# Kernel tuning notes

Hardware: AMD Instinct MI355X
Metric: run time of the kernel (lower is better)

Reference implementation:

```python
import jax, jax.numpy as jnp
import numpy as np

T, D, F, V = 16384, 1024, 2048, 4096


def _mlp(x, w1, w2):
    # residual ReLU MLP stand-in for a transformer stack (tokenwise)
    return x + jax.nn.relu(x @ w1) @ w2


def setup_inputs() -> dict:
    key = jax.random.key(0)
    ks = jax.random.split(key, 11)
    s1 = 1.0 / np.sqrt(D)
    s2 = 1.0 / np.sqrt(F)
    g = lambda k, shape, sc: jax.random.normal(k, shape, dtype=jnp.float32) * sc
    return {
        "inputs_embeds": g(ks[0], (T, D), 1.0),
        "enc_w1": g(ks[1], (D, F), s1),
        "enc_w2": g(ks[2], (F, D), s2),
        "back_w1": g(ks[3], (D, F), s1),
        "back_w2": g(ks[4], (F, D), s2),
        "dec_w1": g(ks[5], (D, F), s1),
        "dec_w2": g(ks[6], (F, D), s2),
        "sp_w": g(ks[7], (D, 1), s1),
        "sp_b": jnp.zeros((1,), jnp.float32),
        "pos_emb": g(ks[8], (T, D), 0.02),
        "lm_head": g(ks[9], (D, V), s1),
        "cu_seq_lens": jnp.array([0, 4096, 8192, 12288, 16384], dtype=jnp.int32),
    }


def reference(inputs_embeds, enc_w1, enc_w2, back_w1, back_w2, dec_w1, dec_w2,
              sp_w, sp_b, pos_emb, lm_head, cu_seq_lens):
    # --- encoder (3-layer stack stand-in) ---
    enc = _mlp(inputs_embeds, enc_w1, enc_w2)                 # [T, D]
    # --- token gate: sigmoid + threshold ---
    w = jax.nn.sigmoid(enc @ sp_w + sp_b)[:, 0]               # [T]
    mask = w >= 0.5                                           # keep mask (= ~zero_mask)
    mi = mask.astype(jnp.int32)
    # --- ragged re-pack: within-segment rank of kept tokens (new position ids) ---
    ecs = jnp.cumsum(mi) - mi                                 # exclusive cumsum of kept
    seg = jnp.searchsorted(cu_seq_lens[1:], jnp.arange(T), side="right")
    base = ecs[cu_seq_lens[:-1]][seg]                         # kept-count before each segment
    new_pos = ecs - base                                      # arange(length) per new segment
    # stable sort places kept tokens first in original (packed) order,
    # exactly matching the per-segment concat of the torch version
    order = jnp.argsort(jnp.logical_not(mask), stable=True)   # [T]
    valid = mask[order]
    # gather + weight by gate value, add new position embedding
    gathered = (enc * w[:, None])[order] + pos_emb[new_pos[order]]
    gathered = jnp.where(valid[:, None], gathered, 0.0)
    # --- backbone compute on packed kept tokens ---
    bb = _mlp(gathered, back_w1, back_w2)                     # [T, D] (padded tail unused)
    # --- scatter-combine: kept slots <- backbone, dropped slots <- encoder residual ---
    inv = jnp.argsort(order)
    combined = jnp.where(mask[:, None], bb[inv], enc)         # [T, D]
    # --- decoder (3-layer stack stand-in) + lm head ---
    dec = _mlp(combined, dec_w1, dec_w2)
    logits = dec @ lm_head                                    # [T, V] fp32
    return logits
```

## Files before the change

kernel.cpp:

```cpp
#include <hip/hip_runtime.h>
#include <hip/hip_bf16.h>
#include <math.h>

static constexpr int TT = 16384;
static constexpr int DD = 1024;
static constexpr int FF = 2048;
static constexpr int VV = 4096;

using bf16 = __hip_bfloat16;
typedef __attribute__((ext_vector_type(8))) short bf16x8;
typedef __attribute__((ext_vector_type(4))) float f32x4;

__device__ inline void gload16(const void* g, void* l) {
    __builtin_amdgcn_global_load_lds(
        (const __attribute__((address_space(1))) void*)g,
        (__attribute__((address_space(3))) void*)l, 16, 0, 0);
}

template<int EPI , bool WB16, bool WF32, bool ROWLIM>
__global__ __launch_bounds__(512, 2)
void mgemm8(const bf16* __restrict__ A, const bf16* __restrict__ BT,
            const float* __restrict__ X, bf16* __restrict__ Ob,
            float* __restrict__ Of,
            int M, int N, int K, const int* __restrict__ rowlim)
{
    if constexpr (ROWLIM) { if ((int)blockIdx.y * 256 >= *rowlim) return; }
    const int m0 = blockIdx.y * 256, n0 = blockIdx.x * 256;

    extern __shared__ char smem[];

    const int tid = threadIdx.x;
    const int wv = tid >> 6, ln = tid & 63;
    const int wm = wv >> 2, wn = wv & 3;
    const int lr = ln & 15, lk = ln >> 4;
    const int swz = (lr & 7) << 4;

    const bf16* Ag = A  + (size_t)m0 * K;
    const bf16* Bg = BT + (size_t)n0 * K;

    const int NT = K >> 6;
    const int NI = NT >> 1;

    const int aoff0 = (wm * 128 + lr) * 128;
    const int boff0 = 32768 + (wn * 64 + lr) * 128;
    const int cb0 = (lk * 16) ^ swz;
    const int cb1 = (64 + lk * 16) ^ swz;

    auto STAGE = [&](const bf16* g, int h, int kt, int buf, int op) {
        const int r = ln >> 3;
        const int c = ((ln & 7) ^ r) * 8;
        const bf16* s = g + (size_t)(h * 128 + wv * 16 + r) * K + kt * 64 + c;
        char* d = smem + buf * 65536 + op * 32768 + h * 16384 + wv * 2048;
        gload16(s, d);
        gload16(s + (size_t)8 * K, d + 1024);
    };
    auto stage_j = [&](int j) {
        const int tile = j >> 2;
        if (tile >= NT) return;
        const int part = j & 3;
        const int buf = tile & 1;
        if (part < 2) STAGE(Bg, part, tile, buf, 1);
        else          STAGE(Ag, part - 2, tile, buf, 0);
    };

    bf16x8 afr[2][2], bfr[4][2];
    f32x4 acc[8][4];
    #pragma unroll
    for (int m = 0; m < 8; ++m)
        #pragma unroll
        for (int n = 0; n < 4; ++n) acc[m][n] = (f32x4){0.f, 0.f, 0.f, 0.f};

#define DS_A(BUF, Q) do {                                                     \
    const char* _p = smem + (BUF) * 65536 + aoff0 + (Q) * 4096;               \
    afr[0][0] = *(const bf16x8*)(_p + cb0);                                   \
    afr[0][1] = *(const bf16x8*)(_p + cb1);                                   \
    afr[1][0] = *(const bf16x8*)(_p + 2048 + cb0);                            \
    afr[1][1] = *(const bf16x8*)(_p + 2048 + cb1);                            \
} while (0)

#define DS_B(BUF) do {                                                        \
    const char* _p = smem + (BUF) * 65536 + boff0;                            \
    _Pragma("unroll")                                                         \
    for (int nf = 0; nf < 4; ++nf) {                                          \
        bfr[nf][0] = *(const bf16x8*)(_p + nf * 2048 + cb0);                  \
        bfr[nf][1] = *(const bf16x8*)(_p + nf * 2048 + cb1);                  \
    }                                                                         \
} while (0)

#define MFMAQ(Q) do {                                                         \
    __builtin_amdgcn_s_setprio(1);                                            \
    _Pragma("unroll")                                                         \
    for (int m2 = 0; m2 < 2; ++m2)                                            \
        _Pragma("unroll")                                                     \
        for (int nf = 0; nf < 4; ++nf) {                                      \
            acc[(Q) * 2 + m2][nf] = __builtin_amdgcn_mfma_f32_16x16x32_bf16(  \
                afr[m2][0], bfr[nf][0], acc[(Q) * 2 + m2][nf], 0, 0, 0);      \
            acc[(Q) * 2 + m2][nf] = __builtin_amdgcn_mfma_f32_16x16x32_bf16(  \
                afr[m2][1], bfr[nf][1], acc[(Q) * 2 + m2][nf], 0, 0, 0);      \
        }                                                                     \
    __builtin_amdgcn_s_setprio(0);                                            \
} while (0)

#define PHASE(Q, BUF, DOB, J, W)                                              \
    {                                                                         \
        DS_A(BUF, Q);                                                         \
        if (DOB) DS_B(BUF);                                                   \
        stage_j(J);                                                           \
        if ((W) == 1)      asm volatile("s_waitcnt vmcnt(6)" ::: "memory");   \
        else if ((W) == 2) asm volatile("s_waitcnt vmcnt(0)" ::: "memory");   \
        __builtin_amdgcn_sched_barrier(0);                                    \
        __builtin_amdgcn_s_barrier();                                         \
        MFMAQ(Q);                                                             \
        __builtin_amdgcn_s_barrier();                                         \
    }

    STAGE(Bg, 0, 0, 0, 1); STAGE(Bg, 1, 0, 0, 1);
    STAGE(Ag, 0, 0, 0, 0); STAGE(Ag, 1, 0, 0, 0);
    asm volatile("s_waitcnt vmcnt(4)" ::: "memory");
    STAGE(Bg, 0, 1, 1, 1); STAGE(Bg, 1, 1, 1, 1);
    STAGE(Ag, 0, 1, 1, 0);
    asm volatile("s_waitcnt vmcnt(6)" ::: "memory");
    __builtin_amdgcn_sched_barrier(0);
    __builtin_amdgcn_s_barrier();

    for (int i = 0; i < NI; ++i) {
        const int jb = 7 + 8 * i;
        const bool last = (i + 1 == NI);
        PHASE(0, 0, true,  jb + 0, 0);
        PHASE(1, 0, false, jb + 1, 0);
        PHASE(2, 0, false, jb + 2, 0);
        PHASE(3, 0, false, jb + 3, last ? 2 : 1);
        PHASE(0, 1, true,  jb + 4, 0);
        PHASE(1, 1, false, jb + 5, 0);
        PHASE(2, 1, false, jb + 6, 0);
        PHASE(3, 1, false, jb + 7, last ? 0 : 1);
    }

#undef PHASE
#undef MFMAQ
#undef DS_B
#undef DS_A

    #pragma unroll
    for (int mf = 0; mf < 8; ++mf)
        #pragma unroll
        for (int nf = 0; nf < 4; ++nf)
            #pragma unroll
            for (int rr = 0; rr < 4; ++rr) {
                const int row = m0 + wm * 128 + mf * 16 + lk * 4 + rr;
                const int col = n0 + wn * 64 + nf * 16 + lr;
                float v = acc[mf][nf][rr];
                if constexpr (EPI == 1) v = fmaxf(v, 0.f);
                if constexpr (EPI == 2) v += X[(size_t)row * N + col];
                if constexpr (WB16) Ob[(size_t)row * N + col] = __float2bfloat16(v);
                if constexpr (WF32) Of[(size_t)row * N + col] = v;
            }
}

__global__ __launch_bounds__(256, 2)
void mgemm_nt3(const bf16* __restrict__ Ah, const bf16* __restrict__ Al,
               const bf16* __restrict__ Bh, const bf16* __restrict__ Bl,
               bf16* __restrict__ Ob, float* __restrict__ gpart,
               const float* __restrict__ qv, int M, int N, int K)
{
    const int m0 = blockIdx.y * 128, n0 = blockIdx.x * 128;

    extern __shared__ char smem[];
    bf16* sAh = (bf16*)smem;
    bf16* sBh = (bf16*)(smem + 8192);
    bf16* sAl = (bf16*)(smem + 16384);
    bf16* sBl = (bf16*)(smem + 24576);

    const int tid = threadIdx.x;
    const int wv = tid >> 6, ln = tid & 63;
    const int wm = wv >> 1, wn = wv & 1;
    const int lr = ln & 15, lk = ln >> 4;
    const int arow = ln >> 2;
    const int acol = (ln & 3) * 8;

    const bf16* Abase_h = Ah + (size_t)m0 * K;
    const bf16* Abase_l = Al + (size_t)m0 * K;
    const bf16* Bbase_h = Bh + (size_t)n0 * K;
    const bf16* Bbase_l = Bl + (size_t)n0 * K;

    f32x4 acc[4][4];
    #pragma unroll
    for (int m = 0; m < 4; ++m)
        #pragma unroll
        for (int n = 0; n < 4; ++n) acc[m][n] = (f32x4){0.f, 0.f, 0.f, 0.f};

    const int nt = K >> 5;
    for (int kt = 0; kt < nt; ++kt) {
        #pragma unroll
        for (int p = 0; p < 2; ++p) {
            const int row = p * 64 + wv * 16;
            gload16(Abase_h + (size_t)(row + arow) * K + kt * 32 + acol, sAh + row * 32);
            gload16(Bbase_h + (size_t)(row + arow) * K + kt * 32 + acol, sBh + row * 32);
            gload16(Abase_l + (size_t)(row + arow) * K + kt * 32 + acol, sAl + row * 32);
            gload16(Bbase_l + (size_t)(row + arow) * K + kt * 32 + acol, sBl + row * 32);
        }
        __syncthreads();

        bf16x8 ah[4], bh[4], al[4], bl[4];
        #pragma unroll
        for (int m = 0; m < 4; ++m) {
            ah[m] = *(const bf16x8*)(sAh + (wm * 64 + m * 16 + lr) * 32 + lk * 8);
            al[m] = *(const bf16x8*)(sAl + (wm * 64 + m * 16 + lr) * 32 + lk * 8);
        }
        #pragma unroll
        for (int n = 0; n < 4; ++n) {
            bh[n] = *(const bf16x8*)(sBh + (wn * 64 + n * 16 + lr) * 32 + lk * 8);
            bl[n] = *(const bf16x8*)(sBl + (wn * 64 + n * 16 + lr) * 32 + lk * 8);
        }
        #pragma unroll
        for (int m = 0; m < 4; ++m)
            #pragma unroll
            for (int n = 0; n < 4; ++n) {
                acc[m][n] = __builtin_amdgcn_mfma_f32_16x16x32_bf16(ah[m], bh[n], acc[m][n], 0, 0, 0);
                acc[m][n] = __builtin_amdgcn_mfma_f32_16x16x32_bf16(ah[m], bl[n], acc[m][n], 0, 0, 0);
                acc[m][n] = __builtin_amdgcn_mfma_f32_16x16x32_bf16(al[m], bh[n], acc[m][n], 0, 0, 0);
            }
        __syncthreads();
    }

    {
        float qvv[4];
        #pragma unroll
        for (int n = 0; n < 4; ++n) qvv[n] = qv[n0 + wn * 64 + n * 16 + lr];
        #pragma unroll
        for (int m = 0; m < 4; ++m)
            #pragma unroll
            for (int r = 0; r < 4; ++r) {
                float s = 0.f;
                #pragma unroll
                for (int n = 0; n < 4; ++n) s += fmaxf(acc[m][n][r], 0.f) * qvv[n];
                s += __shfl_xor(s, 1, 64); s += __shfl_xor(s, 2, 64);
                s += __shfl_xor(s, 4, 64); s += __shfl_xor(s, 8, 64);
                if (lr == 0)
                    gpart[(size_t)(blockIdx.x * 2 + wn) * M + (m0 + wm * 64 + m * 16 + lk * 4 + r)] = s;
            }
    }

    #pragma unroll
    for (int m = 0; m < 4; ++m)
        #pragma unroll
        for (int n = 0; n < 4; ++n)
            #pragma unroll
            for (int r = 0; r < 4; ++r) {
                const int row = m0 + wm * 64 + m * 16 + lk * 4 + r;
                const int col = n0 + wn * 64 + n * 16 + lr;
                Ob[(size_t)row * N + col] = __float2bfloat16(fmaxf(acc[m][n][r], 0.f));
            }
}

template<bool SPLIT>
__global__ void wtrans(const float* __restrict__ W, bf16* __restrict__ Th,
                       bf16* __restrict__ Tl, int R, int C)
{
    __shared__ float tile[32][33];
    const int tx = threadIdx.x & 31, ty = threadIdx.x >> 5;
    const int rb = blockIdx.y * 32, cb = blockIdx.x * 32;
    #pragma unroll
    for (int i = 0; i < 32; i += 8)
        tile[ty + i][tx] = W[(size_t)(rb + ty + i) * C + cb + tx];
    __syncthreads();
    #pragma unroll
    for (int i = 0; i < 32; i += 8) {
        const float v = tile[tx][ty + i];
        const size_t o = (size_t)(cb + ty + i) * R + rb + tx;
        const bf16 h = __float2bfloat16(v);
        Th[o] = h;
        if constexpr (SPLIT) Tl[o] = __float2bfloat16(v - __bfloat162float(h));
    }
}

__global__ void splitx(const float* __restrict__ x, bf16* __restrict__ xh,
                       bf16* __restrict__ xl)
{
    const int i = blockIdx.x * 256 + threadIdx.x;
    const float4 v = ((const float4*)x)[i];
    const float f[4] = {v.x, v.y, v.z, v.w};
    #pragma unroll
    for (int j = 0; j < 4; ++j) {
        const bf16 h = __float2bfloat16(f[j]);
        xh[i * 4 + j] = h;
        xl[i * 4 + j] = __float2bfloat16(f[j] - __bfloat162float(h));
    }
}

__global__ void qvec(const float* __restrict__ w2, const float* __restrict__ sp,
                     float* __restrict__ q)
{
    const int f  = blockIdx.x * 4 + (threadIdx.x >> 6);
    const int ln = threadIdx.x & 63;
    float s = 0.f;
    const float* row = w2 + (size_t)f * DD;
    for (int k = ln; k < DD; k += 64) s += row[k] * sp[k];
    #pragma unroll
    for (int off = 32; off > 0; off >>= 1) s += __shfl_xor(s, off, 64);
    if (ln == 0) q[f] = s;
}

__global__ void gate2(const float* __restrict__ x, const float* __restrict__ spw,
                      const float* __restrict__ spb, const float* __restrict__ gpart,
                      float* __restrict__ w, int* __restrict__ mi)
{
    const int t  = blockIdx.x * 4 + (threadIdx.x >> 6);
    const int ln = threadIdx.x & 63;
    float s = 0.f;
    const float* row = x + (size_t)t * DD;
    for (int k = ln; k < DD; k += 64) s += row[k] * spw[k];
    if (ln < 32) s += gpart[(size_t)ln * TT + t];
    #pragma unroll
    for (int off = 32; off > 0; off >>= 1) s += __shfl_xor(s, off, 64);
    if (ln == 0) {
        const float sg = 1.f / (1.f + expf(-(s + spb[0])));
        w[t]  = sg;
        mi[t] = (sg >= 0.5f) ? 1 : 0;
    }
}

__global__ void scan_kernel(const int* __restrict__ mi, const int* __restrict__ cu,
                            int* __restrict__ ecs, int* __restrict__ meta)
{
    __shared__ int sums[256];
    const int tid  = threadIdx.x;
    const int base = tid * 64;
    int s = 0;
    for (int i = 0; i < 64; ++i) s += mi[base + i];
    sums[tid] = s;
    __syncthreads();
    for (int off = 1; off < 256; off <<= 1) {
        int v = (tid >= off) ? sums[tid - off] : 0;
        __syncthreads();
        sums[tid] += v;
        __syncthreads();
    }
    int run = (tid == 0) ? 0 : sums[tid - 1];
    for (int i = 0; i < 64; ++i) { ecs[base + i] = run; run += mi[base + i]; }
    if (tid == 255) meta[0] = sums[255];
    if (tid < 4) {
        const int idx = cu[tid];
        const int tc = idx >> 6, rem = idx & 63;
        int e = (tc == 0) ? 0 : sums[tc - 1];
        for (int i = 0; i < rem; ++i) e += mi[tc * 64 + i];
        meta[1 + tid] = e;
    }
}

__global__ void pack_kernel(const float* __restrict__ enc, const float* __restrict__ w,
                            const int* __restrict__ mi, const int* __restrict__ ecs,
                            const int* __restrict__ cu, const int* __restrict__ meta,
                            const float* __restrict__ pos_emb,
                            float* __restrict__ Pf, bf16* __restrict__ Pb)
{
    const int t    = blockIdx.x * 4 + (threadIdx.x >> 6);
    const int lane = threadIdx.x & 63;
    if (!mi[t]) return;
    const int e = ecs[t];
    int seg = 0;
    #pragma unroll
    for (int ss = 1; ss < 4; ++ss) if (t >= cu[ss]) seg = ss;
    const int np = e - meta[1 + seg];
    const float wt = w[t];
    const float4* src = (const float4*)(enc + (size_t)t * DD);
    const float4* pe  = (const float4*)(pos_emb + (size_t)np * DD);
    float4* dstf = (float4*)(Pf + (size_t)e * DD);
    bf16*   dstb = Pb + (size_t)e * DD;
    for (int c = lane; c < DD / 4; c += 64) {
        float4 v = src[c], p = pe[c];
        v.x = v.x * wt + p.x; v.y = v.y * wt + p.y;
        v.z = v.z * wt + p.z; v.w = v.w * wt + p.w;
        dstf[c] = v;
        dstb[c * 4 + 0] = __float2bfloat16(v.x);
        dstb[c * 4 + 1] = __float2bfloat16(v.y);
        dstb[c * 4 + 2] = __float2bfloat16(v.z);
        dstb[c * 4 + 3] = __float2bfloat16(v.w);
    }
}

__global__ void combine_kernel(float* __restrict__ ENC, const float* __restrict__ BBf,
                               const int* __restrict__ mi, const int* __restrict__ ecs,
                               bf16* __restrict__ Cb)
{
    const int t    = blockIdx.x * 4 + (threadIdx.x >> 6);
    const int lane = threadIdx.x & 63;
    const bool kept = mi[t] != 0;
    const float4* src = kept ? (const float4*)(BBf + (size_t)ecs[t] * DD)
                             : (const float4*)(ENC + (size_t)t * DD);
    float4* dstf = (float4*)(ENC + (size_t)t * DD);
    bf16*   dstb = Cb + (size_t)t * DD;
    for (int c = lane; c < DD / 4; c += 64) {
        const float4 v = src[c];
        if (kept) dstf[c] = v;
        dstb[c * 4 + 0] = __float2bfloat16(v.x);
        dstb[c * 4 + 1] = __float2bfloat16(v.y);
        dstb[c * 4 + 2] = __float2bfloat16(v.z);
        dstb[c * 4 + 3] = __float2bfloat16(v.w);
    }
}

extern "C" void kernel_launch(void* const* d_in, const int* in_sizes, int n_in,
                              void* d_out, int out_size, void* d_ws, size_t ws_size,
                              hipStream_t stream)
{
    (void)in_sizes; (void)n_in; (void)out_size; (void)ws_size;
    const float* x   = (const float*)d_in[0];
    const float* ew1 = (const float*)d_in[1];
    const float* ew2 = (const float*)d_in[2];
    const float* bw1 = (const float*)d_in[3];
    const float* bw2 = (const float*)d_in[4];
    const float* dw1 = (const float*)d_in[5];
    const float* dw2 = (const float*)d_in[6];
    const float* spw = (const float*)d_in[7];
    const float* spb = (const float*)d_in[8];
    const float* pem = (const float*)d_in[9];
    const float* lmh = (const float*)d_in[10];
    const int*   cu  = (const int*)d_in[11];
    float* out = (float*)d_out;

    (void)hipFuncSetAttribute((const void*)mgemm8<2, false, true, false>,
                              hipFuncAttributeMaxDynamicSharedMemorySize, 131072);
    (void)hipFuncSetAttribute((const void*)mgemm8<1, true, false, true>,
                              hipFuncAttributeMaxDynamicSharedMemorySize, 131072);
    (void)hipFuncSetAttribute((const void*)mgemm8<2, false, true, true>,
                              hipFuncAttributeMaxDynamicSharedMemorySize, 131072);
    (void)hipFuncSetAttribute((const void*)mgemm8<1, true, false, false>,
                              hipFuncAttributeMaxDynamicSharedMemorySize, 131072);
    (void)hipFuncSetAttribute((const void*)mgemm8<2, true, false, false>,
                              hipFuncAttributeMaxDynamicSharedMemorySize, 131072);
    (void)hipFuncSetAttribute((const void*)mgemm8<0, false, true, false>,
                              hipFuncAttributeMaxDynamicSharedMemorySize, 131072);

    char* w = (char*)d_ws;
    auto alloc = [&](size_t bytes) { char* p = w; w += bytes; return p; };
    bf16* ew1hT = (bf16*)alloc((size_t)FF * DD * 2);
    bf16* ew1lT = (bf16*)alloc((size_t)FF * DD * 2);
    bf16* ew2T  = (bf16*)alloc((size_t)DD * FF * 2);
    bf16* bw1T  = (bf16*)alloc((size_t)FF * DD * 2);
    bf16* bw2T  = (bf16*)alloc((size_t)DD * FF * 2);
    bf16* lmhT  = (bf16*)alloc((size_t)VV * DD * 2);
    float* qv   = (float*)alloc((size_t)FF * 4);
    float* GP   = (float*)alloc((size_t)32 * TT * 4);
    float* WG   = (float*)alloc((size_t)TT * 4);
    int*   MI   = (int*)alloc((size_t)TT * 4);
    int*   ECS  = (int*)alloc((size_t)TT * 4);
    int*   META = (int*)alloc(64);
    bf16* Xh    = (bf16*)alloc((size_t)TT * DD * 2);
    bf16* Xl    = (bf16*)alloc((size_t)TT * DD * 2);
    bf16* Hb    = (bf16*)alloc((size_t)TT * FF * 2);
    float* ENC  = (float*)alloc((size_t)TT * DD * 4);
    float* Pf   = (float*)alloc((size_t)TT * DD * 4);
    bf16* Pb    = (bf16*)alloc((size_t)TT * DD * 2);
    bf16* dw1T  = ew1hT;
    bf16* dw2T  = ew1lT;

    const dim3 blk(256);
    const dim3 blk8(512);

    splitx<<<TT * DD / 4 / 256, blk, 0, stream>>>(x, Xh, Xl);
    wtrans<true ><<<dim3(FF / 32, DD / 32), blk, 0, stream>>>(ew1, ew1hT, ew1lT, DD, FF);
    wtrans<false><<<dim3(DD / 32, FF / 32), blk, 0, stream>>>(ew2, ew2T, nullptr, FF, DD);
    wtrans<false><<<dim3(FF / 32, DD / 32), blk, 0, stream>>>(bw1, bw1T, nullptr, DD, FF);
    wtrans<false><<<dim3(DD / 32, FF / 32), blk, 0, stream>>>(bw2, bw2T, nullptr, FF, DD);
    wtrans<false><<<dim3(VV / 32, DD / 32), blk, 0, stream>>>(lmh, lmhT, nullptr, DD, VV);
    qvec<<<FF / 4, blk, 0, stream>>>(ew2, spw, qv);

    mgemm_nt3<<<dim3(FF / 128, TT / 128), blk, 32768, stream>>>(
        Xh, Xl, ew1hT, ew1lT, Hb, GP, qv, TT, FF, DD);

    gate2<<<TT / 4, blk, 0, stream>>>(x, spw, spb, GP, WG, MI);
    scan_kernel<<<1, blk, 0, stream>>>(MI, cu, ECS, META);

    mgemm8<2, false, true, false><<<dim3(DD / 256, TT / 256), blk8, 131072, stream>>>(
        Hb, ew2T, x, nullptr, ENC, TT, DD, FF, nullptr);

    pack_kernel<<<TT / 4, blk, 0, stream>>>(ENC, WG, MI, ECS, cu, META, pem, Pf, Pb);

    wtrans<false><<<dim3(FF / 32, DD / 32), blk, 0, stream>>>(dw1, dw1T, nullptr, DD, FF);
    wtrans<false><<<dim3(DD / 32, FF / 32), blk, 0, stream>>>(dw2, dw2T, nullptr, FF, DD);

    mgemm8<1, true, false, true><<<dim3(FF / 256, TT / 256), blk8, 131072, stream>>>(
        Pb, bw1T, nullptr, Hb, nullptr, TT, FF, DD, META);
    mgemm8<2, false, true, true><<<dim3(DD / 256, TT / 256), blk8, 131072, stream>>>(
        Hb, bw2T, Pf, nullptr, Pf, TT, DD, FF, META);

    combine_kernel<<<TT / 4, blk, 0, stream>>>(ENC, Pf, MI, ECS, Xl);

    mgemm8<1, true, false, false><<<dim3(FF / 256, TT / 256), blk8, 131072, stream>>>(
        Xl, dw1T, nullptr, Hb, nullptr, TT, FF, DD, nullptr);
    mgemm8<2, true, false, false><<<dim3(DD / 256, TT / 256), blk8, 131072, stream>>>(
        Hb, dw2T, ENC, Xh, nullptr, TT, DD, FF, nullptr);

    mgemm8<0, false, true, false><<<dim3(VV / 256, TT / 256), blk8, 131072, stream>>>(
        Xh, lmhT, nullptr, nullptr, out, TT, VV, DD, nullptr);
}
```

Measured before the change: 864.5 us.

## Replace split-bf16 encoder GEMM with plain bf16 plus fp32 fixup near gate threshold

The first encoder GEMM drops the three-MFMA hi/lo split-precision scheme and uses the single-pass bf16 mgemm8 kernel, with the gate partial-sum epilogue moved into mgemm8. Tokens whose gate logit lands within a small margin of zero are recorded through an atomic counter. An fp32 GEMV then recomputes their gate contribution so the keep mask still matches the reference. This removes the split conversion, the extra bf16 buffers and two-thirds of the MFMA work in that GEMM. In exchange it adds the fixup kernels and risks mask mismatches if more than CAP tokens fall inside the margin, or if bf16 error exceeds TAU.

```diff
diff --git a/kernel.cpp b/kernel.cpp
--- a/kernel.cpp
+++ b/kernel.cpp
@@ -6,6 +6,8 @@
 static constexpr int DD = 1024;
 static constexpr int FF = 2048;
 static constexpr int VV = 4096;
+static constexpr int CAP = 4096;
+#define TAU 0.02f
 
 using bf16 = __hip_bfloat16;
 typedef __attribute__((ext_vector_type(8))) short bf16x8;
@@ -17,11 +19,12 @@
         (__attribute__((address_space(3))) void*)l, 16, 0, 0);
 }
 
-template<int EPI , bool WB16, bool WF32, bool ROWLIM>
+template<int EPI , bool WB16, bool WF32, bool ROWLIM, bool GPART>
 __global__ __launch_bounds__(512, 2)
 void mgemm8(const bf16* __restrict__ A, const bf16* __restrict__ BT,
             const float* __restrict__ X, bf16* __restrict__ Ob,
-            float* __restrict__ Of,
+            float* __restrict__ Of, float* __restrict__ gpart,
+            const float* __restrict__ qv,
             int M, int N, int K, const int* __restrict__ rowlim)
 {
     if constexpr (ROWLIM) { if ((int)blockIdx.y * 256 >= *rowlim) return; }
@@ -141,6 +144,25 @@
 #undef DS_B
 #undef DS_A
 
+    if constexpr (GPART) {
+        float qvv[4];
+        #pragma unroll
+        for (int nf = 0; nf < 4; ++nf) qvv[nf] = qv[n0 + wn * 64 + nf * 16 + lr];
+        #pragma unroll
+        for (int mf = 0; mf < 8; ++mf)
+            #pragma unroll
+            for (int rr = 0; rr < 4; ++rr) {
+                float s = 0.f;
+                #pragma unroll
+                for (int nf = 0; nf < 4; ++nf) s += fmaxf(acc[mf][nf][rr], 0.f) * qvv[nf];
+                s += __shfl_xor(s, 1, 64); s += __shfl_xor(s, 2, 64);
+                s += __shfl_xor(s, 4, 64); s += __shfl_xor(s, 8, 64);
+                if (lr == 0)
+                    gpart[(size_t)(blockIdx.x * 4 + wn) * M +
+                          (m0 + wm * 128 + mf * 16 + lk * 4 + rr)] = s;
+            }
+    }
+
     #pragma unroll
     for (int mf = 0; mf < 8; ++mf)
         #pragma unroll
@@ -157,105 +179,8 @@
             }
 }
 
-__global__ __launch_bounds__(256, 2)
-void mgemm_nt3(const bf16* __restrict__ Ah, const bf16* __restrict__ Al,
-               const bf16* __restrict__ Bh, const bf16* __restrict__ Bl,
-               bf16* __restrict__ Ob, float* __restrict__ gpart,
-               const float* __restrict__ qv, int M, int N, int K)
-{
-    const int m0 = blockIdx.y * 128, n0 = blockIdx.x * 128;
-
-    extern __shared__ char smem[];
-    bf16* sAh = (bf16*)smem;
-    bf16* sBh = (bf16*)(smem + 8192);
-    bf16* sAl = (bf16*)(smem + 16384);
-    bf16* sBl = (bf16*)(smem + 24576);
-
-    const int tid = threadIdx.x;
-    const int wv = tid >> 6, ln = tid & 63;
-    const int wm = wv >> 1, wn = wv & 1;
-    const int lr = ln & 15, lk = ln >> 4;
-    const int arow = ln >> 2;
-    const int acol = (ln & 3) * 8;
-
-    const bf16* Abase_h = Ah + (size_t)m0 * K;
-    const bf16* Abase_l = Al + (size_t)m0 * K;
-    const bf16* Bbase_h = Bh + (size_t)n0 * K;
-    const bf16* Bbase_l = Bl + (size_t)n0 * K;
-
-    f32x4 acc[4][4];
-    #pragma unroll
-    for (int m = 0; m < 4; ++m)
-        #pragma unroll
-        for (int n = 0; n < 4; ++n) acc[m][n] = (f32x4){0.f, 0.f, 0.f, 0.f};
-
-    const int nt = K >> 5;
-    for (int kt = 0; kt < nt; ++kt) {
-        #pragma unroll
-        for (int p = 0; p < 2; ++p) {
-            const int row = p * 64 + wv * 16;
-            gload16(Abase_h + (size_t)(row + arow) * K + kt * 32 + acol, sAh + row * 32);
-            gload16(Bbase_h + (size_t)(row + arow) * K + kt * 32 + acol, sBh + row * 32);
-            gload16(Abase_l + (size_t)(row + arow) * K + kt * 32 + acol, sAl + row * 32);
-            gload16(Bbase_l + (size_t)(row + arow) * K + kt * 32 + acol, sBl + row * 32);
-        }
-        __syncthreads();
-
-        bf16x8 ah[4], bh[4], al[4], bl[4];
-        #pragma unroll
-        for (int m = 0; m < 4; ++m) {
-            ah[m] = *(const bf16x8*)(sAh + (wm * 64 + m * 16 + lr) * 32 + lk * 8);
-            al[m] = *(const bf16x8*)(sAl + (wm * 64 + m * 16 + lr) * 32 + lk * 8);
-        }
-        #pragma unroll
-        for (int n = 0; n < 4; ++n) {
-            bh[n] = *(const bf16x8*)(sBh + (wn * 64 + n * 16 + lr) * 32 + lk * 8);
-            bl[n] = *(const bf16x8*)(sBl + (wn * 64 + n * 16 + lr) * 32 + lk * 8);
-        }
-        #pragma unroll
-        for (int m = 0; m < 4; ++m)
-            #pragma unroll
-            for (int n = 0; n < 4; ++n) {
-                acc[m][n] = __builtin_amdgcn_mfma_f32_16x16x32_bf16(ah[m], bh[n], acc[m][n], 0, 0, 0);
-                acc[m][n] = __builtin_amdgcn_mfma_f32_16x16x32_bf16(ah[m], bl[n], acc[m][n], 0, 0, 0);
-                acc[m][n] = __builtin_amdgcn_mfma_f32_16x16x32_bf16(al[m], bh[n], acc[m][n], 0, 0, 0);
-            }
-        __syncthreads();
-    }
-
-    {
-        float qvv[4];
-        #pragma unroll
-        for (int n = 0; n < 4; ++n) qvv[n] = qv[n0 + wn * 64 + n * 16 + lr];
-        #pragma unroll
-        for (int m = 0; m < 4; ++m)
-            #pragma unroll
-            for (int r = 0; r < 4; ++r) {
-                float s = 0.f;
-                #pragma unroll
-                for (int n = 0; n < 4; ++n) s += fmaxf(acc[m][n][r], 0.f) * qvv[n];
-                s += __shfl_xor(s, 1, 64); s += __shfl_xor(s, 2, 64);
-                s += __shfl_xor(s, 4, 64); s += __shfl_xor(s, 8, 64);
-                if (lr == 0)
-                    gpart[(size_t)(blockIdx.x * 2 + wn) * M + (m0 + wm * 64 + m * 16 + lk * 4 + r)] = s;
-            }
-    }
-
-    #pragma unroll
-    for (int m = 0; m < 4; ++m)
-        #pragma unroll
-        for (int n = 0; n < 4; ++n)
-            #pragma unroll
-            for (int r = 0; r < 4; ++r) {
-                const int row = m0 + wm * 64 + m * 16 + lk * 4 + r;
-                const int col = n0 + wn * 64 + n * 16 + lr;
-                Ob[(size_t)row * N + col] = __float2bfloat16(fmaxf(acc[m][n][r], 0.f));
-            }
-}
-
-template<bool SPLIT>
 __global__ void wtrans(const float* __restrict__ W, bf16* __restrict__ Th,
-                       bf16* __restrict__ Tl, int R, int C)
+                       int R, int C)
 {
     __shared__ float tile[32][33];
     const int tx = threadIdx.x & 31, ty = threadIdx.x >> 5;
@@ -265,27 +190,18 @@
         tile[ty + i][tx] = W[(size_t)(rb + ty + i) * C + cb + tx];
     __syncthreads();
     #pragma unroll
-    for (int i = 0; i < 32; i += 8) {
-        const float v = tile[tx][ty + i];
-        const size_t o = (size_t)(cb + ty + i) * R + rb + tx;
-        const bf16 h = __float2bfloat16(v);
-        Th[o] = h;
-        if constexpr (SPLIT) Tl[o] = __float2bfloat16(v - __bfloat162float(h));
-    }
-}
-
-__global__ void splitx(const float* __restrict__ x, bf16* __restrict__ xh,
-                       bf16* __restrict__ xl)
+    for (int i = 0; i < 32; i += 8)
+        Th[(size_t)(cb + ty + i) * R + rb + tx] = __float2bfloat16(tile[tx][ty + i]);
+}
+
+__global__ void castx(const float* __restrict__ x, bf16* __restrict__ xb)
 {
     const int i = blockIdx.x * 256 + threadIdx.x;
     const float4 v = ((const float4*)x)[i];
-    const float f[4] = {v.x, v.y, v.z, v.w};
-    #pragma unroll
-    for (int j = 0; j < 4; ++j) {
-        const bf16 h = __float2bfloat16(f[j]);
-        xh[i * 4 + j] = h;
-        xl[i * 4 + j] = __float2bfloat16(f[j] - __bfloat162float(h));
-    }
+    xb[i * 4 + 0] = __float2bfloat16(v.x);
+    xb[i * 4 + 1] = __float2bfloat16(v.y);
+    xb[i * 4 + 2] = __float2bfloat16(v.z);
+    xb[i * 4 + 3] = __float2bfloat16(v.w);
 }
 
 __global__ void qvec(const float* __restrict__ w2, const float* __restrict__ sp,
@@ -303,18 +219,90 @@
 
 __global__ void gate2(const float* __restrict__ x, const float* __restrict__ spw,
                       const float* __restrict__ spb, const float* __restrict__ gpart,
-                      float* __restrict__ w, int* __restrict__ mi)
+                      float* __restrict__ w, int* __restrict__ mi,
+                      float* __restrict__ sx, int* __restrict__ flags,
+                      int* __restrict__ cnt)
 {
     const int t  = blockIdx.x * 4 + (threadIdx.x >> 6);
     const int ln = threadIdx.x & 63;
     float s = 0.f;
     const float* row = x + (size_t)t * DD;
     for (int k = ln; k < DD; k += 64) s += row[k] * spw[k];
-    if (ln < 32) s += gpart[(size_t)ln * TT + t];
     #pragma unroll
     for (int off = 32; off > 0; off >>= 1) s += __shfl_xor(s, off, 64);
+    float g = (ln < 32) ? gpart[(size_t)ln * TT + t] : 0.f;
+    #pragma unroll
+    for (int off = 32; off > 0; off >>= 1) g += __shfl_xor(g, off, 64);
     if (ln == 0) {
-        const float sg = 1.f / (1.f + expf(-(s + spb[0])));
+        const float logit = s + g + spb[0];
+        const float sg = 1.f / (1.f + expf(-logit));
+        w[t]  = sg;
+        mi[t] = (sg >= 0.5f) ? 1 : 0;
+        sx[t] = s;
+        if (fabsf(logit) < TAU) {
+            const int i = atomicAdd(cnt, 1);
+            if (i < CAP) flags[i] = t;
+        }
+    }
+}
+
+__global__ void fixgemv(const float* __restrict__ x, const float* __restrict__ w1,
+                        const float* __restrict__ qv, const int* __restrict__ flags,
+                        const int* __restrict__ cnt, float* __restrict__ gpf)
+{
+    const int nb = min(*cnt, CAP);
+    const int t0 = blockIdx.y * 16;
+    if (t0 >= nb) return;
+    const int ntk = min(16, nb - t0);
+    const int f = blockIdx.x * 256 + threadIdx.x;
+    const float qf = qv[f];
+    __shared__ float xs[16][64];
+    __shared__ float red[4][16];
+    float acc[16];
+    #pragma unroll
+    for (int tk = 0; tk < 16; ++tk) acc[tk] = 0.f;
+
+    for (int d0 = 0; d0 < DD; d0 += 64) {
+        __syncthreads();
+        for (int i = threadIdx.x; i < 16 * 64; i += 256) {
+            const int tk = i >> 6, dd = i & 63;
+            xs[tk][dd] = (tk < ntk)
+                ? x[(size_t)flags[t0 + tk] * DD + d0 + dd] : 0.f;
+        }
+        __syncthreads();
+        for (int dd = 0; dd < 64; ++dd) {
+            const float wv = w1[(size_t)(d0 + dd) * FF + f];
+            #pragma unroll
+            for (int tk = 0; tk < 16; ++tk) acc[tk] += xs[tk][dd] * wv;
+        }
+    }
+    const int wv_ = threadIdx.x >> 6, ln = threadIdx.x & 63;
+    #pragma unroll
+    for (int tk = 0; tk < 16; ++tk) {
+        float v = fmaxf(acc[tk], 0.f) * qf;
+        #pragma unroll
+        for (int off = 32; off > 0; off >>= 1) v += __shfl_xor(v, off, 64);
+        if (ln == 0) red[wv_][tk] = v;
+    }
+    __syncthreads();
+    if (threadIdx.x < 16)
+        gpf[(size_t)blockIdx.x * CAP + t0 + threadIdx.x] =
+            red[0][threadIdx.x] + red[1][threadIdx.x] +
+            red[2][threadIdx.x] + red[3][threadIdx.x];
+}
+
+__global__ void fixres(const float* __restrict__ sx, const float* __restrict__ spb,
+                       const float* __restrict__ gpf, const int* __restrict__ flags,
+                       const int* __restrict__ cnt, float* __restrict__ w,
+                       int* __restrict__ mi)
+{
+    const int nb = min(*cnt, CAP);
+    for (int i = blockIdx.x * 256 + threadIdx.x; i < nb; i += gridDim.x * 256) {
+        const int t = flags[i];
+        float s = sx[t] + spb[0];
+        #pragma unroll
+        for (int fc = 0; fc < 8; ++fc) s += gpf[(size_t)fc * CAP + i];
+        const float sg = 1.f / (1.f + expf(-s));
         w[t]  = sg;
         mi[t] = (sg >= 0.5f) ? 1 : 0;
     }
@@ -419,79 +407,88 @@
     const int*   cu  = (const int*)d_in[11];
     float* out = (float*)d_out;
 
-    (void)hipFuncSetAttribute((const void*)mgemm8<2, false, true, false>,
-                              hipFuncAttributeMaxDynamicSharedMemorySize, 131072);
-    (void)hipFuncSetAttribute((const void*)mgemm8<1, true, false, true>,
-                              hipFuncAttributeMaxDynamicSharedMemorySize, 131072);
-    (void)hipFuncSetAttribute((const void*)mgemm8<2, false, true, true>,
-                              hipFuncAttributeMaxDynamicSharedMemorySize, 131072);
-    (void)hipFuncSetAttribute((const void*)mgemm8<1, true, false, false>,
-                              hipFuncAttributeMaxDynamicSharedMemorySize, 131072);
-    (void)hipFuncSetAttribute((const void*)mgemm8<2, true, false, false>,
-                              hipFuncAttributeMaxDynamicSharedMemorySize, 131072);
-    (void)hipFuncSetAttribute((const void*)mgemm8<0, false, true, false>,
+    (void)hipFuncSetAttribute((const void*)mgemm8<1, true, false, false, true>,
+                              hipFuncAttributeMaxDynamicSharedMemorySize, 131072);
+    (void)hipFuncSetAttribute((const void*)mgemm8<2, false, true, false, false>,
+                              hipFuncAttributeMaxDynamicSharedMemorySize, 131072);
+    (void)hipFuncSetAttribute((const void*)mgemm8<1, true, false, true, false>,
+                              hipFuncAttributeMaxDynamicSharedMemorySize, 131072);
+    (void)hipFuncSetAttribute((const void*)mgemm8<2, false, true, true, false>,
+                              hipFuncAttributeMaxDynamicSharedMemorySize, 131072);
+    (void)hipFuncSetAttribute((const void*)mgemm8<1, true, false, false, false>,
+                              hipFuncAttributeMaxDynamicSharedMemorySize, 131072);
+    (void)hipFuncSetAttribute((const void*)mgemm8<2, true, false, false, false>,
+                              hipFuncAttributeMaxDynamicSharedMemorySize, 131072);
+    (void)hipFuncSetAttribute((const void*)mgemm8<0, false, true, false, false>,
                               hipFuncAttributeMaxDynamicSharedMemorySize, 131072);
 
     char* w = (char*)d_ws;
     auto alloc = [&](size_t bytes) { char* p = w; w += bytes; return p; };
-    bf16* ew1hT = (bf16*)alloc((size_t)FF * DD * 2);
-    bf16* ew1lT = (bf16*)alloc((size_t)FF * DD * 2);
-    bf16* ew2T  = (bf16*)alloc((size_t)DD * FF * 2);
-    bf16* bw1T  = (bf16*)alloc((size_t)FF * DD * 2);
-    bf16* bw2T  = (bf16*)alloc((size_t)DD * FF * 2);
-    bf16* lmhT  = (bf16*)alloc((size_t)VV * DD * 2);
-    float* qv   = (float*)alloc((size_t)FF * 4);
-    float* GP   = (float*)alloc((size_t)32 * TT * 4);
-    float* WG   = (float*)alloc((size_t)TT * 4);
-    int*   MI   = (int*)alloc((size_t)TT * 4);
-    int*   ECS  = (int*)alloc((size_t)TT * 4);
-    int*   META = (int*)alloc(64);
-    bf16* Xh    = (bf16*)alloc((size_t)TT * DD * 2);
-    bf16* Xl    = (bf16*)alloc((size_t)TT * DD * 2);
-    bf16* Hb    = (bf16*)alloc((size_t)TT * FF * 2);
-    float* ENC  = (float*)alloc((size_t)TT * DD * 4);
-    float* Pf   = (float*)alloc((size_t)TT * DD * 4);
-    bf16* Pb    = (bf16*)alloc((size_t)TT * DD * 2);
-    bf16* dw1T  = ew1hT;
-    bf16* dw2T  = ew1lT;
+    bf16* ew1T = (bf16*)alloc((size_t)FF * DD * 2);
+    bf16* ew2T = (bf16*)alloc((size_t)DD * FF * 2);
+    bf16* bw1T = (bf16*)alloc((size_t)FF * DD * 2);
+    bf16* bw2T = (bf16*)alloc((size_t)DD * FF * 2);
+    bf16* dw1T = (bf16*)alloc((size_t)FF * DD * 2);
+    bf16* dw2T = (bf16*)alloc((size_t)DD * FF * 2);
+    bf16* lmhT = (bf16*)alloc((size_t)VV * DD * 2);
+    float* qv  = (float*)alloc((size_t)FF * 4);
+    float* GP  = (float*)alloc((size_t)32 * TT * 4);
+    float* WG  = (float*)alloc((size_t)TT * 4);
+    int*  MI   = (int*)alloc((size_t)TT * 4);
+    int*  ECS  = (int*)alloc((size_t)TT * 4);
+    int*  META = (int*)alloc(64);
+    float* SX  = (float*)alloc((size_t)TT * 4);
+    int*  FLAGS= (int*)alloc((size_t)CAP * 4);
+    int*  CNT  = (int*)alloc(64);
+    float* GPF = (float*)alloc((size_t)8 * CAP * 4);
+    bf16* Xb   = (bf16*)alloc((size_t)TT * DD * 2);
+    bf16* Hb   = (bf16*)alloc((size_t)TT * FF * 2);
+    float* ENC = (float*)alloc((size_t)TT * DD * 4);
+    float* Pf  = (float*)alloc((size_t)TT * DD * 4);
+    bf16* Pb   = (bf16*)alloc((size_t)TT * DD * 2);
+    bf16* Cb   = Xb;
+    bf16* DECb = Pb;
 
     const dim3 blk(256);
     const dim3 blk8(512);
 
-    splitx<<<TT * DD / 4 / 256, blk, 0, stream>>>(x, Xh, Xl);
-    wtrans<true ><<<dim3(FF / 32, DD / 32), blk, 0, stream>>>(ew1, ew1hT, ew1lT, DD, FF);
-    wtrans<false><<<dim3(DD / 32, FF / 32), blk, 0, stream>>>(ew2, ew2T, nullptr, FF, DD);
-    wtrans<false><<<dim3(FF / 32, DD / 32), blk, 0, stream>>>(bw1, bw1T, nullptr, DD, FF);
-    wtrans<false><<<dim3(DD / 32, FF / 32), blk, 0, stream>>>(bw2, bw2T, nullptr, FF, DD);
-    wtrans<false><<<dim3(VV / 32, DD / 32), blk, 0, stream>>>(lmh, lmhT, nullptr, DD, VV);
+    (void)hipMemsetAsync(CNT, 0, 4, stream);
+
+    castx<<<TT * DD / 4 / 256, blk, 0, stream>>>(x, Xb);
+    wtrans<<<dim3(FF / 32, DD / 32), blk, 0, stream>>>(ew1, ew1T, DD, FF);
+    wtrans<<<dim3(DD / 32, FF / 32), blk, 0, stream>>>(ew2, ew2T, FF, DD);
+    wtrans<<<dim3(FF / 32, DD / 32), blk, 0, stream>>>(bw1, bw1T, DD, FF);
+    wtrans<<<dim3(DD / 32, FF / 32), blk, 0, stream>>>(bw2, bw2T, FF, DD);
+    wtrans<<<dim3(FF / 32, DD / 32), blk, 0, stream>>>(dw1, dw1T, DD, FF);
+    wtrans<<<dim3(DD / 32, FF / 32), blk, 0, stream>>>(dw2, dw2T, FF, DD);
+    wtrans<<<dim3(VV / 32, DD / 32), blk, 0, stream>>>(lmh, lmhT, DD, VV);
     qvec<<<FF / 4, blk, 0, stream>>>(ew2, spw, qv);
 
-    mgemm_nt3<<<dim3(FF / 128, TT / 128), blk, 32768, stream>>>(
-        Xh, Xl, ew1hT, ew1lT, Hb, GP, qv, TT, FF, DD);
-
-    gate2<<<TT / 4, blk, 0, stream>>>(x, spw, spb, GP, WG, MI);
+    mgemm8<1, true, false, false, true><<<dim3(FF / 256, TT / 256), blk8, 131072, stream>>>(
+        Xb, ew1T, nullptr, Hb, nullptr, GP, qv, TT, FF, DD, nullptr);
+
+    gate2<<<TT / 4, blk, 0, stream>>>(x, spw, spb, GP, WG, MI, SX, FLAGS, CNT);
+    fixgemv<<<dim3(8, CAP / 16), blk, 0, stream>>>(x, ew1, qv, FLAGS, CNT, GPF);
+    fixres<<<16, blk, 0, stream>>>(SX, spb, GPF, FLAGS, CNT, WG, MI);
     scan_kernel<<<1, blk, 0, stream>>>(MI, cu, ECS, META);
 
-    mgemm8<2, false, true, false><<<dim3(DD / 256, TT / 256), blk8, 131072, stream>>>(
-        Hb, ew2T, x, nullptr, ENC, TT, DD, FF, nullptr);
+    mgemm8<2, false, true, false, false><<<dim3(DD / 256, TT / 256), blk8, 131072, stream>>>(
+        Hb, ew2T, x, nullptr, ENC, nullptr, nullptr, TT, DD, FF, nullptr);
 
     pack_kernel<<<TT / 4, blk, 0, stream>>>(ENC, WG, MI, ECS, cu, META, pem, Pf, Pb);
 
-    wtrans<false><<<dim3(FF / 32, DD / 32), blk, 0, stream>>>(dw1, dw1T, nullptr, DD, FF);
-    wtrans<false><<<dim3(DD / 32, FF / 32), blk, 0, stream>>>(dw2, dw2T, nullptr, FF, DD);
-
-    mgemm8<1, true, false, true><<<dim3(FF / 256, TT / 256), blk8, 131072, stream>>>(
-        Pb, bw1T, nullptr, Hb, nullptr, TT, FF, DD, META);
-    mgemm8<2, false, true, true><<<dim3(DD / 256, TT / 256), blk8, 131072, stream>>>(
-        Hb, bw2T, Pf, nullptr, Pf, TT, DD, FF, META);
-
-    combine_kernel<<<TT / 4, blk, 0, stream>>>(ENC, Pf, MI, ECS, Xl);
-
-    mgemm8<1, true, false, false><<<dim3(FF / 256, TT / 256), blk8, 131072, stream>>>(
-        Xl, dw1T, nullptr, Hb, nullptr, TT, FF, DD, nullptr);
-    mgemm8<2, true, false, false><<<dim3(DD / 256, TT / 256), blk8, 131072, stream>>>(
-        Hb, dw2T, ENC, Xh, nullptr, TT, DD, FF, nullptr);
-
-    mgemm8<0, false, true, false><<<dim3(VV / 256, TT / 256), blk8, 131072, stream>>>(
-        Xh, lmhT, nullptr, nullptr, out, TT, VV, DD, nullptr);
-}
+    mgemm8<1, true, false, true, false><<<dim3(FF / 256, TT / 256), blk8, 131072, stream>>>(
+        Pb, bw1T, nullptr, Hb, nullptr, nullptr, nullptr, TT, FF, DD, META);
+    mgemm8<2, false, true, true, false><<<dim3(DD / 256, TT / 256), blk8, 131072, stream>>>(
+        Hb, bw2T, Pf, nullptr, Pf, nullptr, nullptr, TT, DD, FF, META);
+
+    combine_kernel<<<TT / 4, blk, 0, stream>>>(ENC, Pf, MI, ECS, Cb);
+
+    mgemm8<1, true, false, false, false><<<dim3(FF / 256, TT / 256), blk8, 131072, stream>>>(
+        Cb, dw1T, nullptr, Hb, nullptr, nullptr, nullptr, TT, FF, DD, nullptr);
+    mgemm8<2, true, false, false, false><<<dim3(DD / 256, TT / 256), blk8, 131072, stream>>>(
+        Hb, dw2T, ENC, DECb, nullptr, nullptr, nullptr, TT, DD, FF, nullptr);
+
+    mgemm8<0, false, true, false, false><<<dim3(VV / 256, TT / 256), blk8, 131072, stream>>>(
+        DECb, lmhT, nullptr, nullptr, out, nullptr, nullptr, TT, VV, DD, nullptr);
+}
```

New measurement: 860.8 us. About the same (-0.4%).
